# Kernel tuning notes

Hardware: AMD Instinct MI355X
Metric: run time of the kernel (lower is better)

## Reference

```python
import jax, jax.numpy as jnp
import numpy as np

PSZ = 3      # patch_size
TOPK = 2     # topk candidates
EPS = 1e-12  # F.normalize eps


def extract_patches(x, psz, stride):
    """Torch unfold-style patch extraction: (B,C,H,W) -> (B, nH*nW, C, psz, psz)."""
    B, C, H, W = x.shape
    nH = (H - psz) // stride + 1
    nW = (W - psz) // stride + 1
    slices = []
    for di in range(psz):          # fixed 3x3 loop, not a data-dim loop
        for dj in range(psz):
            slices.append(x[:, :, di:di + (nH - 1) * stride + 1:stride,
                                  dj:dj + (nW - 1) * stride + 1:stride])
    p = jnp.stack(slices, axis=-1)                      # (B,C,nH,nW,psz*psz)
    p = p.reshape(B, C, nH, nW, psz, psz)
    p = p.transpose(0, 2, 3, 1, 4, 5).reshape(B, nH * nW, C, psz, psz)
    return p


def l2_normalize(x, axis):
    n = jnp.sqrt(jnp.sum(x * x, axis=axis, keepdims=True))
    return x / jnp.maximum(n, EPS)


def setup_inputs() -> dict:
    key = jax.random.key(0)
    k1, k2 = jax.random.split(key)
    pred_style = jax.random.normal(k1, (2, 128, 48, 48), dtype=jnp.float32)
    target_style = jax.random.normal(k2, (2 * TOPK, 128, 48, 48), dtype=jnp.float32)
    return {"pred_style": pred_style, "target_style": target_style}


def reference(pred_style, target_style):
    B = pred_style.shape[0]
    # raw patches (used for the final MSE / gather)
    tp = extract_patches(target_style, PSZ, 1)   # (B*TOPK, nT, C, 3, 3)
    pp = extract_patches(pred_style, PSZ, 1)     # (B, nQ, C, 3, 3)
    nT = tp.shape[1]

    # matching is done on channel-normalized features (F.normalize dim=1 / dim=2)
    p1n = extract_patches(l2_normalize(pred_style, axis=1), PSZ, 1)  # (B,nQ,C,3,3)
    tpn = l2_normalize(tp, axis=2).reshape(B, TOPK, nT, *tp.shape[2:])

    # cosine cross-correlation == conv with candidate patches as filters
    scores = jnp.einsum('bqcij,bkncij->bknq', p1n, tpn)  # (B,TOPK,nT,nQ)->(B,TOPK,nQ) reduce below

    sv = jnp.max(scores, axis=2)      # (B, TOPK, nQ) best value per candidate set
    si = jnp.argmax(scores, axis=2)   # (B, TOPK, nQ) best spatial idx per k
    k_idx = jnp.argmax(sv, axis=1)    # (B, nQ) best k per query position
    spatial = jnp.take_along_axis(si, k_idx[:, None, :], axis=1)[:, 0]  # (B, nQ)

    tpr = tp.reshape(B, TOPK, nT, *tp.shape[2:])
    bi = jnp.arange(B)[:, None]
    gathered = tpr[bi, k_idx, spatial]  # (B, nQ, C, 3, 3)

    return jnp.mean((pp - gathered) ** 2)
```

## Files before the change

### kernel.cpp

```cpp
#include <hip/hip_runtime.h>
#include <hip/hip_bf16.h>

typedef unsigned short u16;
typedef __attribute__((ext_vector_type(8))) short short8;
typedef _Float16 half8 __attribute__((ext_vector_type(8)));
typedef __attribute__((ext_vector_type(4))) float f32x4;
typedef __attribute__((ext_vector_type(4))) unsigned int u32x4;

#define CC    128
#define WW    48
#define HW2   2304
#define NHW   46
#define NQ    2116
#define NPIX  2304
#define DSTRIDE ((size_t)NPIX * NPIX + 64)
#define BATCH 2
#define MT    126
#define NTC   190
#define DTS   200

__device__ __forceinline__ u16 f2bf(float f) {
  union { float f; unsigned u; } x; x.f = f;
  unsigned r = (x.u + 0x7fffu + ((x.u >> 16) & 1u)) >> 16;
  return (u16)r;
}

__global__ __launch_bounds__(256) void k_norm(const float* __restrict__ pred,
                                              const float* __restrict__ targ,
                                              u16* __restrict__ PnT, u16* __restrict__ TnT) {
  const int img = blockIdx.y;
  const int p0  = blockIdx.x * 64;
  const int tid = threadIdx.x;
  const float* src = img < 2 ? pred + (size_t)img * CC * HW2
                             : targ + (size_t)(img - 2) * CC * HW2;
  u16* out = img < 2 ? PnT + (size_t)img * NPIX * CC
                     : TnT + (size_t)(img - 2) * NPIX * CC;

  __shared__ float sT[64][129];
  __shared__ float sInv[64];

  #pragma unroll
  for (int it = 0; it < 32; ++it) {
    int idx = it * 256 + tid;
    int c = idx >> 6, p = idx & 63;
    sT[p][c] = src[(size_t)c * HW2 + p0 + p];
  }
  __syncthreads();
  if (tid < 64) {
    float s = 0.f;
    for (int c = 0; c < CC; ++c) { float v = sT[tid][c]; s += v * v; }
    sInv[tid] = 1.0f / fmaxf(sqrtf(s), 1e-12f);
  }
  __syncthreads();
  #pragma unroll
  for (int it = 0; it < 4; ++it) {
    int cid = it * 256 + tid;
    int p = cid >> 4, g = cid & 15;
    int r = p0 + p;
    int sc = (g & ~7) | ((g & 7) ^ (r & 7));
    float inv = sInv[p];
    unsigned pack[4];
    #pragma unroll
    for (int e = 0; e < 8; ++e) {
      float v = sT[p][sc * 8 + e] * inv;
      if ((e & 1) == 0) pack[e >> 1] = (unsigned)f2bf(v);
      else              pack[e >> 1] |= ((unsigned)f2bf(v)) << 16;
    }
    u32x4 o; o.x = pack[0]; o.y = pack[1]; o.z = pack[2]; o.w = pack[3];
    *reinterpret_cast<u32x4*>(out + (size_t)r * CC + g * 8) = o;
  }
}

__global__ __launch_bounds__(512, 2) void k_pixdotH(const u16* __restrict__ PnT, const u16* __restrict__ TnT,
                                                    u16* __restrict__ H) {
  __shared__ u16 buf[40960];
  u16* sA = buf;
  u16* sB = buf + 16384;
  const int nt = blockIdx.x, mt = blockIdx.y, s = blockIdx.z;
  const int tid = threadIdx.x, lane = tid & 63, wid = tid >> 6;
  const int wm = wid >> 2, wn = wid & 3;
  const int r15 = lane & 15, g16 = lane >> 4;
  const int m0 = mt * MT, n0 = nt * NTC;

  const u16* Ab = PnT + (size_t)(s >> 1) * NPIX * CC;
  const u16* Bb = TnT + (size_t)s * NPIX * CC;
  u16* Hs = H + (size_t)s * DSTRIDE;

  #pragma unroll
  for (int i = 0; i < 4; ++i) {
    int sl = i * 512 + tid;
    int row = m0 + (sl >> 4); row = row < 2303 ? row : 2303;
    __builtin_amdgcn_global_load_lds(
      (const __attribute__((address_space(1))) unsigned*)(Ab + (size_t)row * CC + (sl & 15) * 8),
      (__attribute__((address_space(3))) unsigned*)&sA[sl * 8], 16, 0, 0);
  }
  #pragma unroll
  for (int i = 0; i < 6; ++i) {
    int sl = i * 512 + tid;
    int row = n0 + (sl >> 4); row = row < 2303 ? row : 2303;
    __builtin_amdgcn_global_load_lds(
      (const __attribute__((address_space(1))) unsigned*)(Bb + (size_t)row * CC + (sl & 15) * 8),
      (__attribute__((address_space(3))) unsigned*)&sB[sl * 8], 16, 0, 0);
  }

  f32x4 acc[4][3];
  const f32x4 z4 = {0.f, 0.f, 0.f, 0.f};
  #pragma unroll
  for (int i = 0; i < 4; ++i)
    #pragma unroll
    for (int j = 0; j < 3; ++j) acc[i][j] = z4;

  asm volatile("s_waitcnt vmcnt(0)" ::: "memory");
  __builtin_amdgcn_s_barrier();

  const int arow0 = wm * 64 + r15;
  const int brow0 = wn * 48 + r15;
  #pragma unroll
  for (int ks = 0; ks < 4; ++ks) {
    const int c = ks * 4 + g16;
    short8 af[4], bfv[3];
    #pragma unroll
    for (int mi = 0; mi < 4; ++mi) {
      int row = arow0 + mi * 16;
      int gr = m0 + row;
      af[mi] = *reinterpret_cast<const short8*>(
        &sA[row * 128 + (c >> 3) * 64 + (((c & 7) ^ (gr & 7)) * 8)]);
    }
    #pragma unroll
    for (int ni = 0; ni < 3; ++ni) {
      int row = brow0 + ni * 16;
      int gr = n0 + row;
      bfv[ni] = *reinterpret_cast<const short8*>(
        &sB[row * 128 + (c >> 3) * 64 + (((c & 7) ^ (gr & 7)) * 8)]);
    }
    __builtin_amdgcn_s_setprio(1);
    #pragma unroll
    for (int mi = 0; mi < 4; ++mi)
      #pragma unroll
      for (int ni = 0; ni < 3; ++ni)
        acc[mi][ni] = __builtin_amdgcn_mfma_f32_16x16x32_bf16(af[mi], bfv[ni], acc[mi][ni], 0, 0, 0);
    __builtin_amdgcn_s_setprio(0);
  }

  __syncthreads();
  u16* Dt = buf;
  #pragma unroll
  for (int mi = 0; mi < 4; ++mi)
    #pragma unroll
    for (int ni = 0; ni < 3; ++ni) {
      int col = wn * 48 + ni * 16 + r15;
      #pragma unroll
      for (int rg = 0; rg < 4; ++rg) {
        int row = wm * 64 + mi * 16 + g16 * 4 + rg;
        Dt[row * DTS + col] = __builtin_bit_cast(u16, (_Float16)acc[mi][ni][rg]);
      }
    }
  __syncthreads();

  for (int t = tid; t < 126 * 24; t += 512) {
    int rr = t / 24, c8 = t - rr * 24;
    int grow = m0 + rr;
    if (grow >= 2302) continue;
    int lcol = c8 * 8;
    int lim = NTC - lcol;
    int glim = 2302 - (n0 + lcol);
    lim = lim < glim ? lim : glim;
    if (lim <= 0) continue;
    int base = rr * DTS + lcol;
    half8 a0 = *reinterpret_cast<const half8*>(&Dt[base]);
    half8 b0 = *reinterpret_cast<const half8*>(&Dt[base + DTS]);
    half8 b1 = *reinterpret_cast<const half8*>(&Dt[base + DTS + 8]);
    half8 c0 = *reinterpret_cast<const half8*>(&Dt[base + 2 * DTS]);
    half8 c1 = *reinterpret_cast<const half8*>(&Dt[base + 2 * DTS + 8]);
    half8 s1v = __builtin_shufflevector(b0, b1, 1, 2, 3, 4, 5, 6, 7, 8);
    half8 s2v = __builtin_shufflevector(c0, c1, 2, 3, 4, 5, 6, 7, 8, 9);
    half8 sum = a0 + s1v + s2v;
    u32x4 pk = __builtin_bit_cast(u32x4, sum);
    u16* dst = Hs + (size_t)grow * NPIX + n0 + lcol;
    int nd = lim >= 8 ? 4 : (lim >> 1);
    #pragma unroll
    for (int d = 0; d < 4; ++d)
      if (d < nd) *reinterpret_cast<unsigned*>(dst + 2 * d) = pk[d];
  }
}

__global__ __launch_bounds__(512) void k_stencil(const u16* __restrict__ H,
                                                 const float* __restrict__ pred,
                                                 const float* __restrict__ targ,
                                                 float* __restrict__ msep) {
  const int bid = blockIdx.x;
  const int b = bid >= NQ ? 1 : 0;
  const int orig = bid - b * NQ;
  const int xcd = orig & 7, pos = orig >> 3;
  const int q = (xcd < 4 ? xcd * 265 : 1060 + (xcd - 4) * 264) + pos;

  const int tid = threadIdx.x, lane = tid & 63, wid = tid >> 6;
  const int qy = q / NHW, qx = q - qy * NHW;
  const int qp = qy * WW + qx;

  const _Float16 ninf = __builtin_bit_cast(_Float16, (u16)0xFC00);
  half8 pmax = {ninf, ninf, ninf, ninf, ninf, ninf, ninf, ninf};

  #pragma unroll
  for (int it = 0; it < 2; ++it) {
    int t = it * 512 + tid;
    if (t < 552) {
      int kc = t / 276; int rem = t - kc * 276;
      int ny = rem / 6, cx = rem - ny * 6;
      const u16* Hs = H + (size_t)(b * 2 + kc) * DSTRIDE;
      int colb = ny * 48 + cx * 8;
      half8 t0 = *reinterpret_cast<const half8*>(Hs + (size_t)qp * NPIX + colb);
      half8 t1 = *reinterpret_cast<const half8*>(Hs + (size_t)(qp + 48) * NPIX + colb + 48);
      half8 t2 = *reinterpret_cast<const half8*>(Hs + (size_t)(qp + 96) * NPIX + colb + 96);
      half8 sm = t0 + t1 + t2;
      if (cx == 5) { sm[6] = ninf; sm[7] = ninf; }
      pmax = __builtin_elementwise_max(pmax, sm);
    }
  }
  float m = (float)pmax[0];
  #pragma unroll
  for (int e = 1; e < 8; ++e) { float v = (float)pmax[e]; m = v > m ? v : m; }
  #pragma unroll
  for (int off = 1; off < 64; off <<= 1) {
    float o = __shfl_xor(m, off, 64);
    m = o > m ? o : m;
  }
  __shared__ float sv[8];
  __shared__ int si[8];
  __shared__ float rsum[8];
  if (lane == 0) sv[wid] = m;
  __syncthreads();
  float M = sv[0];
  #pragma unroll
  for (int wv = 1; wv < 8; ++wv) M = sv[wv] > M ? sv[wv] : M;

  int nmin = 0x7fffffff;
  if (m == M) {
    #pragma unroll
    for (int it = 0; it < 2; ++it) {
      int t = it * 512 + tid;
      if (t < 552) {
        int kc = t / 276; int rem = t - kc * 276;
        int ny = rem / 6, cx = rem - ny * 6;
        const u16* Hs = H + (size_t)(b * 2 + kc) * DSTRIDE;
        int colb = ny * 48 + cx * 8;
        half8 t0 = *reinterpret_cast<const half8*>(Hs + (size_t)qp * NPIX + colb);
        half8 t1 = *reinterpret_cast<const half8*>(Hs + (size_t)(qp + 48) * NPIX + colb + 48);
        half8 t2 = *reinterpret_cast<const half8*>(Hs + (size_t)(qp + 96) * NPIX + colb + 96);
        half8 sm = t0 + t1 + t2;
        if (cx == 5) { sm[6] = ninf; sm[7] = ninf; }
        int nbase = kc * NQ + ny * NHW + cx * 8;
        #pragma unroll
        for (int e = 0; e < 8; ++e) {
          float sc = (float)sm[e];
          int n = nbase + e;
          if (sc == M && n < nmin) nmin = n;
        }
      }
    }
  }
  #pragma unroll
  for (int off = 1; off < 64; off <<= 1) {
    int o = __shfl_xor(nmin, off, 64);
    nmin = o < nmin ? o : nmin;
  }
  if (lane == 0) si[wid] = nmin;
  __syncthreads();
  int fi = si[0];
  #pragma unroll
  for (int wv = 1; wv < 8; ++wv) fi = si[wv] < fi ? si[wv] : fi;

  int nkc = fi >= NQ ? 1 : 0;
  int ns = fi - nkc * NQ;
  int ny = ns / NHW, nx = ns - ny * NHW;
  const float* P = pred + (size_t)b * CC * HW2;
  const float* T = targ + (size_t)(b * 2 + nkc) * CC * HW2;
  float ssum = 0.f;
  for (int i = tid; i < CC * 9; i += 512) {
    int c = i / 9, sp = i - 9 * c;
    int di = sp / 3, dj = sp - 3 * di;
    float d = P[(size_t)c * HW2 + (qy + di) * WW + qx + dj]
            - T[(size_t)c * HW2 + (ny + di) * WW + nx + dj];
    ssum += d * d;
  }
  #pragma unroll
  for (int off = 1; off < 64; off <<= 1) ssum += __shfl_xor(ssum, off, 64);
  if (lane == 0) rsum[wid] = ssum;
  __syncthreads();
  if (tid == 0) {
    float t = 0.f;
    #pragma unroll
    for (int wv = 0; wv < 8; ++wv) t += rsum[wv];
    msep[b * NQ + q] = t;
  }
}

__global__ void k_final(const float* __restrict__ msep, float* __restrict__ out) {
  int t = threadIdx.x;
  float s = 0.f;
  for (int i = t; i < BATCH * NQ; i += 256) s += msep[i];
  __shared__ float red[256];
  red[t] = s; __syncthreads();
  for (int st = 128; st > 0; st >>= 1) { if (t < st) red[t] += red[t + st]; __syncthreads(); }
  if (t == 0) out[0] = red[0] * (1.0f / 4875264.0f);
}

extern "C" void kernel_launch(void* const* d_in, const int* in_sizes, int n_in,
                              void* d_out, int out_size, void* d_ws, size_t ws_size,
                              hipStream_t stream) {
  const float* pred = (const float*)d_in[0];
  const float* targ = (const float*)d_in[1];
  char* ws = (char*)d_ws;

  size_t offP = 0;
  size_t offT = offP + (size_t)2 * NPIX * CC * 2;
  size_t offH = offT + (size_t)4 * NPIX * CC * 2;
  size_t offM = offH + (size_t)4 * DSTRIDE * 2;

  u16*   PnT  = (u16*)(ws + offP);
  u16*   TnT  = (u16*)(ws + offT);
  u16*   Hbuf = (u16*)(ws + offH);
  float* msep = (float*)(ws + offM);

  k_norm<<<dim3(36, 6), 256, 0, stream>>>(pred, targ, PnT, TnT);
  k_pixdotH<<<dim3(13, 19, 4), 512, 0, stream>>>(PnT, TnT, Hbuf);
  k_stencil<<<dim3(BATCH * NQ), 512, 0, stream>>>(Hbuf, pred, targ, msep);
  k_final<<<1, 256, 0, stream>>>(msep, (float*)d_out);
}
```

Measured before the change: 70.24 us.

## Process two query positions per stencil block and cache window sums in registers

Each 512-thread stencil block now handles two adjacent query positions, 256 threads each, and the grid is halved. The XCD swizzle is rebuilt around query pairs. Each thread keeps its three computed window-sum vectors and their base indices in registers, so the argmin pass no longer re-reads H from memory. This removes half the H global traffic and block scheduling overhead, at the cost of more registers per thread. A clamp on the spatial index was added as a safeguard.

New measurement: 67.39 us. 4.1% less time.

```diff
diff --git a/kernel.cpp b/kernel.cpp
--- a/kernel.cpp
+++ b/kernel.cpp
@@ -189,21 +189,30 @@
                                                  const float* __restrict__ targ,
                                                  float* __restrict__ msep) {
   const int bid = blockIdx.x;
-  const int b = bid >= NQ ? 1 : 0;
-  const int orig = bid - b * NQ;
-  const int xcd = orig & 7, pos = orig >> 3;
-  const int q = (xcd < 4 ? xcd * 265 : 1060 + (xcd - 4) * 264) + pos;
-
-  const int tid = threadIdx.x, lane = tid & 63, wid = tid >> 6;
+  const int b = bid >= 1058 ? 1 : 0;
+  const int j = bid - b * 1058;
+  const int xcd = j & 7, pos = j >> 3;
+  const int jswz = (xcd < 2 ? xcd * 133 : 266 + (xcd - 2) * 132) + pos;
+
+  const int tid = threadIdx.x;
+  const int hid = tid >> 8, htid = tid & 255;
+  const int lane = tid & 63, wid = tid >> 6;
+  const int q = jswz * 2 + hid;
   const int qy = q / NHW, qx = q - qy * NHW;
   const int qp = qy * WW + qx;
 
   const _Float16 ninf = __builtin_bit_cast(_Float16, (u16)0xFC00);
-  half8 pmax = {ninf, ninf, ninf, ninf, ninf, ninf, ninf, ninf};
-
-  #pragma unroll
-  for (int it = 0; it < 2; ++it) {
-    int t = it * 512 + tid;
+  const half8 ninf8 = {ninf, ninf, ninf, ninf, ninf, ninf, ninf, ninf};
+
+  half8 smc[3];
+  int nb[3];
+  smc[0] = ninf8; smc[1] = ninf8; smc[2] = ninf8;
+  nb[0] = nb[1] = nb[2] = 0;
+
+  half8 pmax = ninf8;
+  #pragma unroll
+  for (int it = 0; it < 3; ++it) {
+    int t = it * 256 + htid;
     if (t < 552) {
       int kc = t / 276; int rem = t - kc * 276;
       int ny = rem / 6, cx = rem - ny * 6;
@@ -214,6 +223,8 @@
       half8 t2 = *reinterpret_cast<const half8*>(Hs + (size_t)(qp + 96) * NPIX + colb + 96);
       half8 sm = t0 + t1 + t2;
       if (cx == 5) { sm[6] = ninf; sm[7] = ninf; }
+      smc[it] = sm;
+      nb[it] = kc * NQ + ny * NHW + cx * 8;
       pmax = __builtin_elementwise_max(pmax, sm);
     }
   }
@@ -230,32 +241,19 @@
   __shared__ float rsum[8];
   if (lane == 0) sv[wid] = m;
   __syncthreads();
-  float M = sv[0];
-  #pragma unroll
-  for (int wv = 1; wv < 8; ++wv) M = sv[wv] > M ? sv[wv] : M;
+  float M = sv[hid * 4];
+  #pragma unroll
+  for (int wv = 1; wv < 4; ++wv) { float v = sv[hid * 4 + wv]; M = v > M ? v : M; }
 
   int nmin = 0x7fffffff;
   if (m == M) {
     #pragma unroll
-    for (int it = 0; it < 2; ++it) {
-      int t = it * 512 + tid;
-      if (t < 552) {
-        int kc = t / 276; int rem = t - kc * 276;
-        int ny = rem / 6, cx = rem - ny * 6;
-        const u16* Hs = H + (size_t)(b * 2 + kc) * DSTRIDE;
-        int colb = ny * 48 + cx * 8;
-        half8 t0 = *reinterpret_cast<const half8*>(Hs + (size_t)qp * NPIX + colb);
-        half8 t1 = *reinterpret_cast<const half8*>(Hs + (size_t)(qp + 48) * NPIX + colb + 48);
-        half8 t2 = *reinterpret_cast<const half8*>(Hs + (size_t)(qp + 96) * NPIX + colb + 96);
-        half8 sm = t0 + t1 + t2;
-        if (cx == 5) { sm[6] = ninf; sm[7] = ninf; }
-        int nbase = kc * NQ + ny * NHW + cx * 8;
-        #pragma unroll
-        for (int e = 0; e < 8; ++e) {
-          float sc = (float)sm[e];
-          int n = nbase + e;
-          if (sc == M && n < nmin) nmin = n;
-        }
+    for (int it = 0; it < 3; ++it) {
+      #pragma unroll
+      for (int e = 0; e < 8; ++e) {
+        float sc = (float)smc[it][e];
+        int n = nb[it] + e;
+        if (sc == M && n < nmin) nmin = n;
       }
     }
   }
@@ -266,17 +264,18 @@
   }
   if (lane == 0) si[wid] = nmin;
   __syncthreads();
-  int fi = si[0];
-  #pragma unroll
-  for (int wv = 1; wv < 8; ++wv) fi = si[wv] < fi ? si[wv] : fi;
+  int fi = si[hid * 4];
+  #pragma unroll
+  for (int wv = 1; wv < 4; ++wv) { int v = si[hid * 4 + wv]; fi = v < fi ? v : fi; }
 
   int nkc = fi >= NQ ? 1 : 0;
   int ns = fi - nkc * NQ;
+  ns = ns < NQ ? ns : NQ - 1;
   int ny = ns / NHW, nx = ns - ny * NHW;
   const float* P = pred + (size_t)b * CC * HW2;
   const float* T = targ + (size_t)(b * 2 + nkc) * CC * HW2;
   float ssum = 0.f;
-  for (int i = tid; i < CC * 9; i += 512) {
+  for (int i = htid; i < CC * 9; i += 256) {
     int c = i / 9, sp = i - 9 * c;
     int di = sp / 3, dj = sp - 3 * di;
     float d = P[(size_t)c * HW2 + (qy + di) * WW + qx + dj]
@@ -287,10 +286,10 @@
   for (int off = 1; off < 64; off <<= 1) ssum += __shfl_xor(ssum, off, 64);
   if (lane == 0) rsum[wid] = ssum;
   __syncthreads();
-  if (tid == 0) {
+  if (htid == 0) {
     float t = 0.f;
     #pragma unroll
-    for (int wv = 0; wv < 8; ++wv) t += rsum[wv];
+    for (int wv = 0; wv < 4; ++wv) t += rsum[hid * 4 + wv];
     msep[b * NQ + q] = t;
   }
 }
@@ -324,6 +323,6 @@
 
   k_norm<<<dim3(36, 6), 256, 0, stream>>>(pred, targ, PnT, TnT);
   k_pixdotH<<<dim3(13, 19, 4), 512, 0, stream>>>(PnT, TnT, Hbuf);
-  k_stencil<<<dim3(BATCH * NQ), 512, 0, stream>>>(Hbuf, pred, targ, msep);
+  k_stencil<<<dim3(2 * 1058), 512, 0, stream>>>(Hbuf, pred, targ, msep);
   k_final<<<1, 256, 0, stream>>>(msep, (float*)d_out);
 }
```
